# Kernel tuning notes

Measured on AMD Instinct MI355X. Metric: run time of the kernel, lower is better.

Reference implementation:

```python
import jax, jax.numpy as jnp
import numpy as np

GROUP_SIZE = 128
N_BITS = 4
QMAX = 2 ** N_BITS - 1
NUM_EXPERTS = 8
HIDDEN = 2048
INTER = 768
NUM_ROT = 4
T_TOKENS = 4096
TOP_K = 2


def _make_pairs(rng, n_rot, in_feat):
    # intra-group permutation per rotation (valid disjoint Givens pairs)
    n_groups = in_feat // GROUP_SIZE
    return np.stack([
        np.concatenate([rng.permutation(GROUP_SIZE) for _ in range(n_groups)])
        for _ in range(n_rot)
    ]).astype(np.int32)


def _round_ste(x):
    return x + jax.lax.stop_gradient(jnp.round(x) - x)


def _rotate(W, pairs, angles):
    # W: [N, in_feat]; pairs: [R, in_feat] intra-group perm; angles: [R, in_feat//2]
    in_feat = W.shape[1]
    base = (jnp.arange(in_feat) // GROUP_SIZE) * GROUP_SIZE
    for r in range(pairs.shape[0]):
        abs_idx = base + pairs[r]
        i_idx = abs_idx[0::2]
        j_idx = abs_idx[1::2]
        c = jnp.cos(angles[r])
        s = jnp.sin(angles[r])
        wi = W[:, i_idx]
        wj = W[:, j_idx]
        W = W.at[:, i_idx].set(c * wi - s * wj).at[:, j_idx].set(s * wi + c * wj)
    return W


def _fake_quant(W):
    # groupwise asymmetric min-max fake quantization with STE rounding
    shape = W.shape
    wg = W.reshape(-1, GROUP_SIZE)
    wmax = wg.max(axis=-1, keepdims=True)
    wmin = wg.min(axis=-1, keepdims=True)
    scale = jnp.clip(wmax - wmin, 1e-5, None) / QMAX
    zero = jnp.round(-wmin / scale)
    q = jnp.clip(_round_ste(wg / scale) + zero, 0.0, float(QMAX))
    return ((q - zero) * scale).reshape(shape)


def _pseudo_quantize(W3, pairs, angles, ch_scales):
    # scale -> rotate -> fake-quant -> inverse rotate (reversed order, -angles) -> unscale
    E, O, In = W3.shape
    W = W3.reshape(-1, In) * ch_scales
    W = _rotate(W, pairs, angles)
    W = _fake_quant(W)
    W = _rotate(W, pairs[::-1], -angles[::-1])
    return (W / ch_scales).reshape(E, O, In)


def setup_inputs() -> dict:
    key = jax.random.key(0)
    ks = jax.random.split(key, 8)
    rng = np.random.default_rng(0)
    hidden_states = jax.random.normal(ks[0], (T_TOKENS, HIDDEN), jnp.float32)
    top_k_index = jax.random.randint(ks[1], (T_TOKENS, TOP_K), 0, NUM_EXPERTS, jnp.int32)
    logits = jax.random.normal(ks[2], (T_TOKENS, TOP_K), jnp.float32)
    top_k_weights = jax.nn.softmax(logits, axis=-1)
    gate_up_weight = jax.random.normal(ks[3], (NUM_EXPERTS, 2 * INTER, HIDDEN), jnp.float32) * 0.02
    down_weight = jax.random.normal(ks[4], (NUM_EXPERTS, HIDDEN, INTER), jnp.float32) * 0.02
    gate_up_pairs = jnp.asarray(_make_pairs(rng, NUM_ROT, HIDDEN))
    down_pairs = jnp.asarray(_make_pairs(rng, NUM_ROT, INTER))
    gate_up_angles = jax.random.normal(ks[5], (NUM_ROT, HIDDEN // 2), jnp.float32) * 0.1
    down_angles = jax.random.normal(ks[6], (NUM_ROT, INTER // 2), jnp.float32) * 0.1
    k7, k8 = jax.random.split(ks[7])
    gate_up_channel_scales = jax.random.uniform(k7, (1, HIDDEN), jnp.float32, 0.5, 1.5)
    down_channel_scales = jax.random.uniform(k8, (1, INTER), jnp.float32, 0.5, 1.5)
    return {
        "hidden_states": hidden_states,
        "top_k_index": top_k_index,
        "top_k_weights": top_k_weights,
        "gate_up_weight": gate_up_weight,
        "down_weight": down_weight,
        "gate_up_pairs": gate_up_pairs,
        "gate_up_angles": gate_up_angles,
        "down_pairs": down_pairs,
        "down_angles": down_angles,
        "gate_up_channel_scales": gate_up_channel_scales,
        "down_channel_scales": down_channel_scales,
    }


def reference(hidden_states, top_k_index, top_k_weights, gate_up_weight, down_weight,
              gate_up_pairs, gate_up_angles, down_pairs, down_angles,
              gate_up_channel_scales, down_channel_scales):
    # dequantize expert weights
    gup = _pseudo_quantize(gate_up_weight, gate_up_pairs, gate_up_angles, gate_up_channel_scales)  # [E,2I,H]
    dwn = _pseudo_quantize(down_weight, down_pairs, down_angles, down_channel_scales)              # [E,H,I]
    T = hidden_states.shape[0]
    E = gup.shape[0]
    # dense dispatch: all experts for all tokens (E small), combined by routing weights
    h = jnp.einsum('th,eoh->teo', hidden_states, gup)          # [T,E,2I]
    gate, up = jnp.split(h, 2, axis=-1)
    inter = jax.nn.silu(gate) * up                              # [T,E,I]
    y = jnp.einsum('tei,ehi->teh', inter, dwn)                  # [T,E,H]
    combine = jnp.zeros((T, E), hidden_states.dtype)
    combine = combine.at[jnp.arange(T)[:, None], top_k_index].add(top_k_weights)
    return jnp.einsum('teh,te->th', y, combine)
```

## Files before the change

### kernel.cpp

```cpp
#include <hip/hip_runtime.h>

#define T_TOKENS 4096
#define HIDDEN   2048
#define INTERM   768
#define NE       8
#define NPAIR    8192
#define NROT     4
#define MAXT     72

typedef __bf16 bf16x8 __attribute__((ext_vector_type(8)));
typedef float  f32x4  __attribute__((ext_vector_type(4)));

__device__ __forceinline__ unsigned short f2bf(float f) {
  unsigned u = __float_as_uint(f);
  u += 0x7fffu + ((u >> 16) & 1u);
  return (unsigned short)(u >> 16);
}

__device__ __forceinline__ void async16(const void* g, void* l) {
  __builtin_amdgcn_global_load_lds((const __attribute__((address_space(1))) void*)g,
                                   (__attribute__((address_space(3))) void*)l, 16, 0, 0);
}

__global__ void k_hist(const int* __restrict__ idx, int* __restrict__ cnt) {
  const int t = blockIdx.x * 256 + threadIdx.x;
  if (t < NPAIR) atomicAdd(&cnt[idx[t]], 1);
}

__global__ void k_scan(const int* __restrict__ cnt, int* __restrict__ off,
                       int* __restrict__ cur, int* __restrict__ tmap,
                       int* __restrict__ nv) {
  if (threadIdx.x == 0) {
    int a = 0, tt = 0;
    for (int e = 0; e < NE; ++e) {
      off[e] = a; cur[e] = 0;
      const int c = cnt[e];
      for (int m = 0; m < c; m += 128) tmap[tt++] = (e << 16) | (m >> 7);
      a += c;
    }
    nv[0] = tt;
    for (; tt < MAXT; ++tt) tmap[tt] = -1;
  }
}

__global__ void k_scatter(const int* __restrict__ idx, const float* __restrict__ wts,
                          const int* __restrict__ off, int* __restrict__ cur,
                          int* __restrict__ pt, float* __restrict__ pw) {
  const int t = blockIdx.x * 256 + threadIdx.x;
  if (t < NPAIR) {
    const int e = idx[t];
    const int pos = off[e] + atomicAdd(&cur[e], 1);
    pt[pos] = t;
    pw[pos] = wts[t];
  }
}

__global__ void k_tbl(const int* __restrict__ gp, const float* __restrict__ ga,
                      const int* __restrict__ dp, const float* __restrict__ da,
                      const float* __restrict__ gch, const float* __restrict__ dch,
                      float4* __restrict__ tg, float4* __restrict__ td,
                      float* __restrict__ grch, float* __restrict__ drch) {
  const int t = blockIdx.x * 256 + threadIdx.x;
  if (t < NROT * (HIDDEN / 2)) {
    const int r = t >> 10, s = t & 1023;
    const int grp = s >> 6;
    const int i = gp[r * HIDDEN + 2 * s], j = gp[r * HIDDEN + 2 * s + 1];
    const float a = ga[r * (HIDDEN / 2) + s];
    const float c = cosf(a), sn = sinf(a);
    tg[(grp * NROT + r) * 128 + i] = make_float4(c, -sn, __int_as_float(j), 0.f);
    tg[(grp * NROT + r) * 128 + j] = make_float4(c,  sn, __int_as_float(i), 0.f);
  }
  if (t < NROT * (INTERM / 2)) {
    const int r = t / (INTERM / 2), s = t - r * (INTERM / 2);
    const int grp = s >> 6;
    const int i = dp[r * INTERM + 2 * s], j = dp[r * INTERM + 2 * s + 1];
    const float a = da[r * (INTERM / 2) + s];
    const float c = cosf(a), sn = sinf(a);
    td[(grp * NROT + r) * 128 + i] = make_float4(c, -sn, __int_as_float(j), 0.f);
    td[(grp * NROT + r) * 128 + j] = make_float4(c,  sn, __int_as_float(i), 0.f);
  }
  if (t < HIDDEN) grch[t] = 1.0f / gch[t];
  if (t < INTERM) drch[t] = 1.0f / dch[t];
}

#define FWD_ROT(tl, v0, v1)                                                     \
  _Pragma("unroll")                                                             \
  for (int r = 0; r < NROT; ++r) {                                              \
    const float4 e0 = tl[r * 128 + l];                                          \
    const float4 e1 = tl[r * 128 + 64 + l];                                     \
    const int p0 = __float_as_int(e0.z), p1 = __float_as_int(e1.z);             \
    const int a0 = (p0 & 63) << 2, a1 = (p1 & 63) << 2;                         \
    _Pragma("unroll")                                                           \
    for (int q = 0; q < 4; ++q) {                                               \
      const int x0 = __float_as_int(v0[q]), x1 = __float_as_int(v1[q]);         \
      const float lo0 = __int_as_float(__builtin_amdgcn_ds_bpermute(a0, x0));   \
      const float hi0 = __int_as_float(__builtin_amdgcn_ds_bpermute(a0, x1));   \
      const float lo1 = __int_as_float(__builtin_amdgcn_ds_bpermute(a1, x0));   \
      const float hi1 = __int_as_float(__builtin_amdgcn_ds_bpermute(a1, x1));   \
      const float op0 = (p0 & 64) ? hi0 : lo0;                                  \
      const float op1 = (p1 & 64) ? hi1 : lo1;                                  \
      {                                                                         \
        _Pragma("clang fp contract(off)")                                       \
        v0[q] = e0.x * v0[q] + e0.y * op0;                                      \
        v1[q] = e1.x * v1[q] + e1.y * op1;                                      \
      }                                                                         \
    }                                                                           \
  }

__global__ __launch_bounds__(256) void k_quant(
    const float* __restrict__ W, const float4* __restrict__ tbl,
    const float* __restrict__ ch, unsigned short* __restrict__ out, int In, int G) {
  __shared__ float4 tl[NROT * 128];
  const int wv = threadIdx.x >> 6, l = threadIdx.x & 63;
  const int g = blockIdx.x % G;
  const int rowblk = blockIdx.x / G;
  const int row0 = rowblk * 16 + wv * 4;
  const int colbase = g << 7;
  tl[threadIdx.x]       = tbl[(size_t)g * NROT * 128 + threadIdx.x];
  tl[256 + threadIdx.x] = tbl[(size_t)g * NROT * 128 + 256 + threadIdx.x];
  __syncthreads();
  const float c0 = ch[colbase + l], c1 = ch[colbase + 64 + l];
  float v0[4], v1[4];
#pragma unroll
  for (int q = 0; q < 4; ++q) {
#pragma clang fp contract(off)
    const float* Wr = W + (size_t)(row0 + q) * In + colbase;
    v0[q] = Wr[l] * c0;
    v1[q] = Wr[64 + l] * c1;
  }
  FWD_ROT(tl, v0, v1)
#pragma unroll
  for (int q = 0; q < 4; ++q) {
    float mn = fminf(v0[q], v1[q]), mx = fmaxf(v0[q], v1[q]);
#pragma unroll
    for (int o = 32; o > 0; o >>= 1) {
      mn = fminf(mn, __shfl_xor(mn, o));
      mx = fmaxf(mx, __shfl_xor(mx, o));
    }
    {
#pragma clang fp contract(off)
      const float scale = fmaxf(mx - mn, 1e-5f) / 15.0f;
      const float zero = rintf(-mn / scale);
      const float q0 = fminf(fmaxf(rintf(v0[q] / scale) + zero, 0.0f), 15.0f);
      const float q1 = fminf(fmaxf(rintf(v1[q] / scale) + zero, 0.0f), 15.0f);
      v0[q] = (q0 - zero) * scale;
      v1[q] = (q1 - zero) * scale;
    }
  }
#pragma unroll
  for (int q = 0; q < 4; ++q) {
    unsigned short* Or = out + (size_t)(row0 + q) * In + colbase;
    Or[l]      = f2bf(v0[q]);
    Or[64 + l] = f2bf(v1[q]);
  }
}

__global__ __launch_bounds__(256) void k_rotx(
    const float* __restrict__ X, const float* __restrict__ rch,
    const float4* __restrict__ tbl, unsigned short* __restrict__ out) {
  __shared__ float4 tl[NROT * 128];
  const int wv = threadIdx.x >> 6, l = threadIdx.x & 63;
  const int g = blockIdx.x % 16;
  const int rowblk = blockIdx.x / 16;
  const int row0 = rowblk * 16 + wv * 4;
  const int colbase = g << 7;
  tl[threadIdx.x]       = tbl[(size_t)g * NROT * 128 + threadIdx.x];
  tl[256 + threadIdx.x] = tbl[(size_t)g * NROT * 128 + 256 + threadIdx.x];
  __syncthreads();
  const float i0 = rch[colbase + l], i1 = rch[colbase + 64 + l];
  float v0[4], v1[4];
#pragma unroll
  for (int q = 0; q < 4; ++q) {
    const float* Xr = X + (size_t)(row0 + q) * HIDDEN + colbase;
    v0[q] = Xr[l] * i0;
    v1[q] = Xr[64 + l] * i1;
  }
  FWD_ROT(tl, v0, v1)
#pragma unroll
  for (int q = 0; q < 4; ++q) {
    unsigned short* Or = out + (size_t)(row0 + q) * HIDDEN + colbase;
    Or[l]      = f2bf(v0[q]);
    Or[64 + l] = f2bf(v1[q]);
  }
}

__global__ __launch_bounds__(256) void k_silu2(
    const float* __restrict__ h, const float* __restrict__ pw,
    const float* __restrict__ rch, const float4* __restrict__ tbl,
    unsigned short* __restrict__ out) {
  __shared__ float4 tl[NROT * 128];
  const int wv = threadIdx.x >> 6, l = threadIdx.x & 63;
  const int g = blockIdx.x % 6;
  const int rowblk = blockIdx.x / 6;
  const int row0 = rowblk * 16 + wv * 4;
  const int colbase = g << 7;
  tl[threadIdx.x]       = tbl[(size_t)g * NROT * 128 + threadIdx.x];
  tl[256 + threadIdx.x] = tbl[(size_t)g * NROT * 128 + 256 + threadIdx.x];
  __syncthreads();
  const float i0 = rch[colbase + l], i1 = rch[colbase + 64 + l];
  float v0[4], v1[4];
#pragma unroll
  for (int q = 0; q < 4; ++q) {
    const int row = row0 + q;
    const float wgt = pw[row];
    const float* hr = h + (size_t)row * 1536 + colbase;
    const float g0 = hr[l], g1 = hr[64 + l];
    const float u0 = hr[768 + l], u1 = hr[768 + 64 + l];
    v0[q] = g0 / (1.0f + expf(-g0)) * u0 * wgt * i0;
    v1[q] = g1 / (1.0f + expf(-g1)) * u1 * wgt * i1;
  }
  FWD_ROT(tl, v0, v1)
#pragma unroll
  for (int q = 0; q < 4; ++q) {
    unsigned short* Or = out + (size_t)(row0 + q) * INTERM + colbase;
    Or[l]      = f2bf(v0[q]);
    Or[64 + l] = f2bf(v1[q]);
  }
}

template <int MODE>
__launch_bounds__(256, 3)
__global__ void k_gemm(const unsigned short* __restrict__ A,
                       const unsigned short* __restrict__ Bw,
                       float* __restrict__ C,
                       const int* __restrict__ pt,
                       const int* __restrict__ off,
                       const int* __restrict__ cnt,
                       const int* __restrict__ tmap,
                       const int* __restrict__ nv) {
  constexpr int K = MODE ? INTERM : HIDDEN;
  constexpr int N = MODE ? HIDDEN : 2 * INTERM;
  constexpr int XW = MODE ? 16 : 12;

  const int hw  = blockIdx.x + XW * blockIdx.y;
  const int xcd = hw & 7;
  const int pos = hw >> 3;
  const int nvalid = nv[0];
  const int q8 = nvalid >> 3, r8 = nvalid & 7;
  const int rs = q8 + (xcd < r8 ? 1 : 0);
  const int y0 = xcd * q8 + (xcd < r8 ? xcd : r8);
  if (pos >= rs * XW) return;
  int xg, yg;
  if (MODE == 1) {
    xg = pos & 15; yg = y0 + (pos >> 4);
  } else {
    const int cap6 = rs * 6;
    const int half = (pos >= cap6) ? 1 : 0;
    const int rem  = pos - half * cap6;
    xg = half * 6 + rem % 6;
    yg = y0 + rem / 6;
  }
  const int tm = tmap[yg];
  if (tm < 0) return;
  const int e = tm >> 16;
  const int m0 = (tm & 0xffff) << 7;
  const int count = cnt[e];
  const int seg = off[e];
  const int n0 = xg * 128;
  const unsigned short* Be = Bw + (size_t)e * N * K;

  __shared__ unsigned short As[3][128 * 32];
  __shared__ unsigned short Bs[3][128 * 32];

  const int tid = threadIdx.x;
  const int w = tid >> 6;
  const int l = tid & 63;
  const int r0 = w * 16 + (l >> 2);
  const int r1 = r0 + 64;
  const int kco = (l & 3) * 8;

  int p0 = m0 + r0; if (p0 > count - 1) p0 = count - 1;
  int p1 = m0 + r1; if (p1 > count - 1) p1 = count - 1;
  size_t arow0, arow1;
  if (MODE == 0) { arow0 = (size_t)(pt[seg + p0] >> 1); arow1 = (size_t)(pt[seg + p1] >> 1); }
  else           { arow0 = (size_t)(seg + p0); arow1 = (size_t)(seg + p1); }
  const unsigned short* pa0 = A + arow0 * K + kco;
  const unsigned short* pa1 = A + arow1 * K + kco;
  const unsigned short* pb0 = Be + (size_t)(n0 + r0) * K + kco;
  const unsigned short* pb1 = Be + (size_t)(n0 + r1) * K + kco;

  const int ko = (l >> 4) * 8;
  const int mrow = (w & 1) * 64 + (l & 15);
  const int nrow = (w >> 1) * 64 + (l & 15);

  f32x4 acc[4][4];
#pragma unroll
  for (int i = 0; i < 4; ++i)
#pragma unroll
    for (int j = 0; j < 4; ++j) acc[i][j] = (f32x4)0.0f;

#define STAGE(b, kn) do {                              \
    async16(pa0 + (kn), &As[b][w * 512]);              \
    async16(pa1 + (kn), &As[b][(w + 4) * 512]);        \
    async16(pb0 + (kn), &Bs[b][w * 512]);              \
    async16(pb1 + (kn), &Bs[b][(w + 4) * 512]);        \
  } while (0)

  STAGE(0, 0);
  STAGE(1, 32);

  int buf = 0;
  for (int k0 = 0; k0 < K; k0 += 32) {
    asm volatile("s_waitcnt lgkmcnt(0)" ::: "memory");
    if (k0 + 32 < K) asm volatile("s_waitcnt vmcnt(4)" ::: "memory");
    else             asm volatile("s_waitcnt vmcnt(0)" ::: "memory");
    __builtin_amdgcn_s_barrier();
    __builtin_amdgcn_sched_barrier(0);
    const int kn = k0 + 64;
    if (kn < K) {
      const int nb3 = (buf == 0) ? 2 : buf - 1;
      STAGE(nb3, kn);
    }
    bf16x8 af[4], bfr[4];
#pragma unroll
    for (int i = 0; i < 4; ++i)
      af[i] = *(const bf16x8*)&As[buf][(mrow + i * 16) * 32 + ko];
#pragma unroll
    for (int j = 0; j < 4; ++j)
      bfr[j] = *(const bf16x8*)&Bs[buf][(nrow + j * 16) * 32 + ko];
#pragma unroll
    for (int i = 0; i < 4; ++i)
#pragma unroll
      for (int j = 0; j < 4; ++j)
        acc[i][j] = __builtin_amdgcn_mfma_f32_16x16x32_bf16(af[i], bfr[j], acc[i][j], 0, 0, 0);
    buf = (buf == 2) ? 0 : buf + 1;
  }
#undef STAGE

  const int mb = (w & 1) * 64 + (l >> 4) * 4;
  const int nb = n0 + (w >> 1) * 64 + (l & 15);
#pragma unroll
  for (int i = 0; i < 4; ++i) {
#pragma unroll
    for (int j = 0; j < 4; ++j) {
#pragma unroll
      for (int r = 0; r < 4; ++r) {
        const int mm = m0 + mb + i * 16 + r;
        if (mm < count) {
          const int nn = nb + j * 16;
          if (MODE == 0) {
            C[(size_t)(seg + mm) * N + nn] = acc[i][j][r];
          } else {
            C[(size_t)pt[seg + mm] * N + nn] = acc[i][j][r];
          }
        }
      }
    }
  }
}

__global__ __launch_bounds__(256) void k_combine(const float4* __restrict__ y,
                                                 float4* __restrict__ out) {
  const int t = blockIdx.x;
  const float4* y0 = y + (size_t)(2 * t) * (HIDDEN / 4);
  const float4* y1 = y + (size_t)(2 * t + 1) * (HIDDEN / 4);
  float4* o = out + (size_t)t * (HIDDEN / 4);
#pragma unroll
  for (int q = 0; q < 2; ++q) {
    const int c = threadIdx.x + q * 256;
    const float4 a = y0[c], b = y1[c];
    o[c] = make_float4(a.x + b.x, a.y + b.y, a.z + b.z, a.w + b.w);
  }
}

extern "C" void kernel_launch(void* const* d_in, const int* in_sizes, int n_in,
                              void* d_out, int out_size, void* d_ws, size_t ws_size,
                              hipStream_t stream) {
  const float* hs  = (const float*)d_in[0];
  const int*   tki = (const int*)d_in[1];
  const float* tkw = (const float*)d_in[2];
  const float* guw = (const float*)d_in[3];
  const float* dww = (const float*)d_in[4];
  const int*   gupr= (const int*)d_in[5];
  const float* gua = (const float*)d_in[6];
  const int*   dwp = (const int*)d_in[7];
  const float* dwa = (const float*)d_in[8];
  const float* gus = (const float*)d_in[9];
  const float* dwsc= (const float*)d_in[10];
  float* out = (float*)d_out;
  char* ws = (char*)d_ws;

  unsigned short* gup_bf = (unsigned short*)(ws + 0);
  unsigned short* dwn_bf = (unsigned short*)(ws + 50331648);
  unsigned short* x_bf   = (unsigned short*)(ws + 75497472);
  float*          hbuf   = (float*)(ws + 92274688);
  unsigned short* interb = (unsigned short*)(ws + 142606336);
  float*          ybuf   = (float*)(ws + 75497472);
  int*            pt     = (int*)(ws + 155189248);
  float*          pw     = (float*)(ws + 155222016);
  int*            cnt    = (int*)(ws + 155254784);
  int*            off    = cnt + 8;
  int*            cur    = cnt + 16;
  int*            tmap   = cnt + 24;
  int*            nv     = cnt + 120;
  float4*         tg     = (float4*)(ws + 155258880);
  float4*         td     = (float4*)(ws + 155389952);
  float*          grch   = (float*)(ws + 155439104);
  float*          drch   = (float*)(ws + 155447296);

  (void)hipMemsetAsync(cnt, 0, 32, stream);

  k_hist<<<32, 256, 0, stream>>>(tki, cnt);
  k_scan<<<1, 64, 0, stream>>>(cnt, off, cur, tmap, nv);
  k_scatter<<<32, 256, 0, stream>>>(tki, tkw, off, cur, pt, pw);
  k_tbl<<<16, 256, 0, stream>>>(gupr, gua, dwp, dwa, gus, dwsc, tg, td, grch, drch);
  k_rotx<<<4096, 256, 0, stream>>>(hs, grch, tg, x_bf);
  k_quant<<<12288, 256, 0, stream>>>(guw, tg, gus, gup_bf, HIDDEN, 16);
  k_quant<<<6144, 256, 0, stream>>>(dww, td, dwsc, dwn_bf, INTERM, 6);
  k_gemm<0><<<dim3(12, MAXT), 256, 0, stream>>>(x_bf, gup_bf, hbuf, pt, off, cnt, tmap, nv);
  k_silu2<<<3072, 256, 0, stream>>>(hbuf, pw, drch, td, interb);
  k_gemm<1><<<dim3(16, MAXT), 256, 0, stream>>>(interb, dwn_bf, ybuf, pt, off, cnt, tmap, nv);
  k_combine<<<T_TOKENS, 256, 0, stream>>>((const float4*)ybuf, (float4*)out);
}
```

Before: 558.7 us.

## Enlarge grouped GEMM tiles to 256x256 with 8-wave ping-pong pipeline

Both grouped expert GEMMs move from 128x128 tiles with 4 waves to 256x256 tiles with 8 waves, and the tile map now steps per 256 tokens. The K loop uses 64-wide steps split into four MFMA phases with interleaved async LDS staging, XOR-swizzled LDS layout, and setprio around the MFMA bursts. The aim is higher arithmetic intensity and fewer redundant global loads per FLOP. The cost is more padding waste on partial expert segments, fewer blocks to fill the CUs, and heavier register and LDS use per block.

```diff
diff --git a/kernel.cpp b/kernel.cpp
--- a/kernel.cpp
+++ b/kernel.cpp
@@ -6,7 +6,7 @@
 #define NE       8
 #define NPAIR    8192
 #define NROT     4
-#define MAXT     72
+#define MAXT     40
 
 typedef __bf16 bf16x8 __attribute__((ext_vector_type(8)));
 typedef float  f32x4  __attribute__((ext_vector_type(4)));
@@ -35,7 +35,7 @@
     for (int e = 0; e < NE; ++e) {
       off[e] = a; cur[e] = 0;
       const int c = cnt[e];
-      for (int m = 0; m < c; m += 128) tmap[tt++] = (e << 16) | (m >> 7);
+      for (int m = 0; m < c; m += 256) tmap[tt++] = (e << 16) | (m >> 8);
       a += c;
     }
     nv[0] = tt;
@@ -219,7 +219,7 @@
 }
 
 template <int MODE>
-__launch_bounds__(256, 3)
+__launch_bounds__(512, 2)
 __global__ void k_gemm(const unsigned short* __restrict__ A,
                        const unsigned short* __restrict__ Bw,
                        float* __restrict__ C,
@@ -230,7 +230,8 @@
                        const int* __restrict__ nv) {
   constexpr int K = MODE ? INTERM : HIDDEN;
   constexpr int N = MODE ? HIDDEN : 2 * INTERM;
-  constexpr int XW = MODE ? 16 : 12;
+  constexpr int XW = MODE ? 8 : 6;
+  constexpr int NT = K / 64;
 
   const int hw  = blockIdx.x + XW * blockIdx.y;
   const int xcd = hw & 7;
@@ -240,97 +241,140 @@
   const int rs = q8 + (xcd < r8 ? 1 : 0);
   const int y0 = xcd * q8 + (xcd < r8 ? xcd : r8);
   if (pos >= rs * XW) return;
-  int xg, yg;
-  if (MODE == 1) {
-    xg = pos & 15; yg = y0 + (pos >> 4);
-  } else {
-    const int cap6 = rs * 6;
-    const int half = (pos >= cap6) ? 1 : 0;
-    const int rem  = pos - half * cap6;
-    xg = half * 6 + rem % 6;
-    yg = y0 + rem / 6;
-  }
+  const int xg = pos % XW;
+  const int yg = y0 + pos / XW;
   const int tm = tmap[yg];
   if (tm < 0) return;
   const int e = tm >> 16;
-  const int m0 = (tm & 0xffff) << 7;
+  const int m0 = (tm & 0xffff) << 8;
   const int count = cnt[e];
   const int seg = off[e];
-  const int n0 = xg * 128;
+  const int n0 = xg * 256;
   const unsigned short* Be = Bw + (size_t)e * N * K;
 
-  __shared__ unsigned short As[3][128 * 32];
-  __shared__ unsigned short Bs[3][128 * 32];
+  __shared__ unsigned short lds[65536];
 
   const int tid = threadIdx.x;
-  const int w = tid >> 6;
-  const int l = tid & 63;
-  const int r0 = w * 16 + (l >> 2);
-  const int r1 = r0 + 64;
-  const int kco = (l & 3) * 8;
-
-  int p0 = m0 + r0; if (p0 > count - 1) p0 = count - 1;
-  int p1 = m0 + r1; if (p1 > count - 1) p1 = count - 1;
+  const int w = tid >> 6, l = tid & 63;
+  const int wm = w >> 2, wn = w & 3;
+  const int w512 = w * 512;
+
+  const int sr = tid >> 2;
+  const int cs = (((tid & 3) ^ (sr & 3))) * 8;
+  int pA0 = m0 + sr;        if (pA0 > count - 1) pA0 = count - 1;
+  int pA1 = m0 + sr + 128;  if (pA1 > count - 1) pA1 = count - 1;
   size_t arow0, arow1;
-  if (MODE == 0) { arow0 = (size_t)(pt[seg + p0] >> 1); arow1 = (size_t)(pt[seg + p1] >> 1); }
-  else           { arow0 = (size_t)(seg + p0); arow1 = (size_t)(seg + p1); }
-  const unsigned short* pa0 = A + arow0 * K + kco;
-  const unsigned short* pa1 = A + arow1 * K + kco;
-  const unsigned short* pb0 = Be + (size_t)(n0 + r0) * K + kco;
-  const unsigned short* pb1 = Be + (size_t)(n0 + r1) * K + kco;
-
-  const int ko = (l >> 4) * 8;
-  const int mrow = (w & 1) * 64 + (l & 15);
-  const int nrow = (w >> 1) * 64 + (l & 15);
-
-  f32x4 acc[4][4];
-#pragma unroll
-  for (int i = 0; i < 4; ++i)
+  if (MODE == 0) { arow0 = (size_t)(pt[seg + pA0] >> 1); arow1 = (size_t)(pt[seg + pA1] >> 1); }
+  else           { arow0 = (size_t)(seg + pA0); arow1 = (size_t)(seg + pA1); }
+  const unsigned short* paS0 = A + arow0 * K + cs;
+  const unsigned short* paS1 = A + arow1 * K + cs;
+  const unsigned short* pbS0 = Be + (size_t)(n0 + sr) * K + cs;
+  const unsigned short* pbS1 = Be + (size_t)(n0 + sr + 128) * K + cs;
+
+  const int cswz  = ((l >> 4) ^ (l & 3)) * 8;
+  const int abase = (wm * 128 + (l & 15)) * 32 + cswz;
+  const int bbase = (wn * 64  + (l & 15)) * 32 + cswz + 16384;
+
+  f32x4 acc[8][4];
+#pragma unroll
+  for (int i = 0; i < 8; ++i)
 #pragma unroll
     for (int j = 0; j < 4; ++j) acc[i][j] = (f32x4)0.0f;
 
-#define STAGE(b, kn) do {                              \
-    async16(pa0 + (kn), &As[b][w * 512]);              \
-    async16(pa1 + (kn), &As[b][(w + 4) * 512]);        \
-    async16(pb0 + (kn), &Bs[b][w * 512]);              \
-    async16(pb1 + (kn), &Bs[b][(w + 4) * 512]);        \
-  } while (0)
-
-  STAGE(0, 0);
-  STAGE(1, 32);
-
-  int buf = 0;
-  for (int k0 = 0; k0 < K; k0 += 32) {
+#define STG_A(dst, koff) do { \
+    async16(paS0 + (koff), &lds[(dst) + w512]); \
+    async16(paS1 + (koff), &lds[(dst) + 4096 + w512]); } while (0)
+#define STG_B(dst, koff) do { \
+    async16(pbS0 + (koff), &lds[(dst) + w512]); \
+    async16(pbS1 + (koff), &lds[(dst) + 4096 + w512]); } while (0)
+
+  STG_A(0,     0);  STG_B(16384,       0);
+  STG_A(8192,  32); STG_B(16384+8192,  32);
+  STG_A(32768, 64); STG_B(32768+16384, 64);
+  asm volatile("s_waitcnt vmcnt(4)" ::: "memory");
+  __builtin_amdgcn_s_barrier();
+
+  for (int t = 0; t < NT; ++t) {
+    const int base = (t & 1) << 15;
+    const int alt  = base ^ 32768;
+    const int k1 = (t + 1) * 64, k2 = (t + 2) * 64;
+    bf16x8 a[4], bq[4];
+
+#pragma unroll
+    for (int ii = 0; ii < 4; ++ii) a[ii]  = *(const bf16x8*)&lds[base + abase + ii * 512];
+#pragma unroll
+    for (int j = 0; j < 4; ++j)    bq[j]  = *(const bf16x8*)&lds[base + bbase + j * 512];
+    if (t + 1 < NT) STG_A(alt + 8192, k1 + 32);
+    __builtin_amdgcn_s_barrier();
     asm volatile("s_waitcnt lgkmcnt(0)" ::: "memory");
-    if (k0 + 32 < K) asm volatile("s_waitcnt vmcnt(4)" ::: "memory");
-    else             asm volatile("s_waitcnt vmcnt(0)" ::: "memory");
-    __builtin_amdgcn_s_barrier();
     __builtin_amdgcn_sched_barrier(0);
-    const int kn = k0 + 64;
-    if (kn < K) {
-      const int nb3 = (buf == 0) ? 2 : buf - 1;
-      STAGE(nb3, kn);
+    __builtin_amdgcn_s_setprio(1);
+#pragma unroll
+    for (int ii = 0; ii < 4; ++ii)
+#pragma unroll
+      for (int j = 0; j < 4; ++j)
+        acc[ii][j] = __builtin_amdgcn_mfma_f32_16x16x32_bf16(a[ii], bq[j], acc[ii][j], 0, 0, 0);
+    __builtin_amdgcn_s_setprio(0);
+    __builtin_amdgcn_s_barrier();
+
+#pragma unroll
+    for (int ii = 0; ii < 4; ++ii) a[ii] = *(const bf16x8*)&lds[base + abase + (4 + ii) * 512];
+    if (t + 1 < NT) STG_B(alt + 16384 + 8192, k1 + 32);
+    __builtin_amdgcn_s_barrier();
+    asm volatile("s_waitcnt lgkmcnt(0)" ::: "memory");
+    __builtin_amdgcn_sched_barrier(0);
+    __builtin_amdgcn_s_setprio(1);
+#pragma unroll
+    for (int ii = 0; ii < 4; ++ii)
+#pragma unroll
+      for (int j = 0; j < 4; ++j)
+        acc[4 + ii][j] = __builtin_amdgcn_mfma_f32_16x16x32_bf16(a[ii], bq[j], acc[4 + ii][j], 0, 0, 0);
+    __builtin_amdgcn_s_setprio(0);
+    __builtin_amdgcn_s_barrier();
+
+#pragma unroll
+    for (int ii = 0; ii < 4; ++ii) a[ii] = *(const bf16x8*)&lds[base + 8192 + abase + ii * 512];
+#pragma unroll
+    for (int j = 0; j < 4; ++j)    bq[j] = *(const bf16x8*)&lds[base + 8192 + bbase + j * 512];
+    if (t + 2 < NT) STG_A(base, k2);
+    __builtin_amdgcn_s_barrier();
+    asm volatile("s_waitcnt lgkmcnt(0)" ::: "memory");
+    __builtin_amdgcn_sched_barrier(0);
+    __builtin_amdgcn_s_setprio(1);
+#pragma unroll
+    for (int ii = 0; ii < 4; ++ii)
+#pragma unroll
+      for (int j = 0; j < 4; ++j)
+        acc[ii][j] = __builtin_amdgcn_mfma_f32_16x16x32_bf16(a[ii], bq[j], acc[ii][j], 0, 0, 0);
+    __builtin_amdgcn_s_setprio(0);
+    __builtin_amdgcn_s_barrier();
+
+#pragma unroll
+    for (int ii = 0; ii < 4; ++ii) a[ii] = *(const bf16x8*)&lds[base + 8192 + abase + (4 + ii) * 512];
+    if (t + 2 < NT) STG_B(base + 16384, k2);
+    __builtin_amdgcn_s_barrier();
+    asm volatile("s_waitcnt lgkmcnt(0)" ::: "memory");
+    __builtin_amdgcn_sched_barrier(0);
+    __builtin_amdgcn_s_setprio(1);
+#pragma unroll
+    for (int ii = 0; ii < 4; ++ii)
+#pragma unroll
+      for (int j = 0; j < 4; ++j)
+        acc[4 + ii][j] = __builtin_amdgcn_mfma_f32_16x16x32_bf16(a[ii], bq[j], acc[4 + ii][j], 0, 0, 0);
+    __builtin_amdgcn_s_setprio(0);
+    if (t + 1 < NT) {
+      if (t + 1 == NT - 1) asm volatile("s_waitcnt vmcnt(0)" ::: "memory");
+      else                 asm volatile("s_waitcnt vmcnt(4)" ::: "memory");
     }
-    bf16x8 af[4], bfr[4];
-#pragma unroll
-    for (int i = 0; i < 4; ++i)
-      af[i] = *(const bf16x8*)&As[buf][(mrow + i * 16) * 32 + ko];
-#pragma unroll
-    for (int j = 0; j < 4; ++j)
-      bfr[j] = *(const bf16x8*)&Bs[buf][(nrow + j * 16) * 32 + ko];
-#pragma unroll
-    for (int i = 0; i < 4; ++i)
-#pragma unroll
-      for (int j = 0; j < 4; ++j)
-        acc[i][j] = __builtin_amdgcn_mfma_f32_16x16x32_bf16(af[i], bfr[j], acc[i][j], 0, 0, 0);
-    buf = (buf == 2) ? 0 : buf + 1;
-  }
-#undef STAGE
-
-  const int mb = (w & 1) * 64 + (l >> 4) * 4;
-  const int nb = n0 + (w >> 1) * 64 + (l & 15);
-#pragma unroll
-  for (int i = 0; i < 4; ++i) {
+    __builtin_amdgcn_s_barrier();
+  }
+#undef STG_A
+#undef STG_B
+
+  const int mb = wm * 128 + (l >> 4) * 4;
+  const int nb = n0 + wn * 64 + (l & 15);
+#pragma unroll
+  for (int i = 0; i < 8; ++i) {
 #pragma unroll
     for (int j = 0; j < 4; ++j) {
 #pragma unroll
@@ -407,8 +451,8 @@
   k_rotx<<<4096, 256, 0, stream>>>(hs, grch, tg, x_bf);
   k_quant<<<12288, 256, 0, stream>>>(guw, tg, gus, gup_bf, HIDDEN, 16);
   k_quant<<<6144, 256, 0, stream>>>(dww, td, dwsc, dwn_bf, INTERM, 6);
-  k_gemm<0><<<dim3(12, MAXT), 256, 0, stream>>>(x_bf, gup_bf, hbuf, pt, off, cnt, tmap, nv);
+  k_gemm<0><<<dim3(6, MAXT), 512, 0, stream>>>(x_bf, gup_bf, hbuf, pt, off, cnt, tmap, nv);
   k_silu2<<<3072, 256, 0, stream>>>(hbuf, pw, drch, td, interb);
-  k_gemm<1><<<dim3(16, MAXT), 256, 0, stream>>>(interb, dwn_bf, ybuf, pt, off, cnt, tmap, nv);
+  k_gemm<1><<<dim3(8, MAXT), 512, 0, stream>>>(interb, dwn_bf, ybuf, pt, off, cnt, tmap, nv);
   k_combine<<<T_TOKENS, 256, 0, stream>>>((const float4*)ybuf, (float4*)out);
 }
```

Measured after the change: 548.4 us. About the same (-1.8%).
